# Kernel tuning notes

Hardware: AMD Instinct MI355X
Metric: run time of the kernel (lower is better)

Reference implementation:

```python
import jax, jax.numpy as jnp
import numpy as np

D_MODEL = 1024
NUM_HEADS = 16
THETA = 10000.0


def _rope(x, positions):
    # x: [..., S, d_k] with interleaved even/odd pairs; positions: [S] int
    d_k = x.shape[-1]
    inv_freq = 1.0 / (THETA ** (jnp.arange(0, d_k, 2, dtype=jnp.float32) / d_k))  # [d_k/2]
    freqs = positions.astype(jnp.float32)[:, None] * inv_freq[None, :]  # [S, d_k/2]
    cos = jnp.cos(freqs)
    sin = jnp.sin(freqs)
    x_even = x[..., 0::2]
    x_odd = x[..., 1::2]
    rot_even = x_even * cos - x_odd * sin
    rot_odd = x_even * sin + x_odd * cos
    out = jnp.stack([rot_even, rot_odd], axis=-1)  # [..., S, d_k/2, 2]
    return out.reshape(x.shape)


def setup_inputs() -> dict:
    key = jax.random.key(0)
    k1, k2, k3 = jax.random.split(key, 3)
    B, S = 2, 2048
    x = jax.random.normal(k1, (B, S, D_MODEL), dtype=jnp.float32)
    Wqkv = jax.random.normal(k2, (3 * D_MODEL, D_MODEL), dtype=jnp.float32) * (D_MODEL ** -0.5)
    Wout = jax.random.normal(k3, (D_MODEL, D_MODEL), dtype=jnp.float32) * (D_MODEL ** -0.5)
    token_positions = jnp.arange(S, dtype=jnp.int32)
    return {"x": x, "Wqkv": Wqkv, "Wout": Wout, "token_positions": token_positions}


def reference(x, Wqkv, Wout, token_positions):
    B, S, D = x.shape
    H = NUM_HEADS
    d_k = D // H
    qkv = x @ Wqkv.T  # [B, S, 3D]
    qkv = qkv.reshape(B, S, 3, H, d_k).transpose(0, 2, 3, 1, 4)  # [B, 3, H, S, d_k]
    q, k, v = qkv[:, 0], qkv[:, 1], qkv[:, 2]  # each [B, H, S, d_k]
    q = _rope(q, token_positions)
    k = _rope(k, token_positions)
    scores = jnp.einsum("bhqd,bhkd->bhqk", q, k) / jnp.sqrt(jnp.float32(d_k))
    attn = jax.nn.softmax(scores, axis=-1)
    out = jnp.einsum("bhqk,bhkd->bhqd", attn, v)  # [B, H, S, d_k]
    out = out.transpose(0, 2, 1, 3).reshape(B, S, D)
    return out @ Wout.T
```

## Files before the change

kernel.cpp:

```cpp
#include <hip/hip_runtime.h>
#include <stdint.h>

typedef unsigned short u16;
typedef unsigned int u32;
typedef __bf16 bf16x8 __attribute__((ext_vector_type(8)));
typedef float f32x4 __attribute__((ext_vector_type(4)));
typedef float f32x16 __attribute__((ext_vector_type(16)));

#define MFMA16 __builtin_amdgcn_mfma_f32_16x16x32_bf16
#define MFMA32 __builtin_amdgcn_mfma_f32_32x32x16_bf16

static __device__ __forceinline__ u16 f2bf(float f) {
  union { float f; u32 u; } v; v.f = f;
  u32 r = v.u + 0x7FFFu + ((v.u >> 16) & 1u);
  return (u16)(r >> 16);
}
static __device__ __forceinline__ float bf2f(u16 b) {
  union { float f; u32 u; } v; v.u = ((u32)b) << 16;
  return v.f;
}
static __device__ __forceinline__ void load_lds16(const void* g, void* l) {
  __builtin_amdgcn_global_load_lds(
      (const __attribute__((address_space(1))) void*)g,
      (__attribute__((address_space(3))) void*)l, 16, 0, 0);
}

__global__ __launch_bounds__(256) void cvt_bf16(const float* __restrict__ in,
                                                u16* __restrict__ out, int n4) {
  int i = blockIdx.x * 256 + threadIdx.x;
  if (i >= n4) return;
  float4 v = reinterpret_cast<const float4*>(in)[i];
  uint2 r;
  r.x = (u32)f2bf(v.x) | ((u32)f2bf(v.y) << 16);
  r.y = (u32)f2bf(v.z) | ((u32)f2bf(v.w) << 16);
  reinterpret_cast<uint2*>(out)[i] = r;
}

template <bool OUT_BF16>
__global__ __launch_bounds__(256, 2) void gemm_bt(const u16* __restrict__ A,
                                                  const u16* __restrict__ B,
                                                  void* __restrict__ Cv,
                                                  int M, int N, int K) {
  __shared__ u16 As[128 * 32];
  __shared__ u16 Bs[128 * 32];
  const int t = threadIdx.x;
  const int w = t >> 6, lane = t & 63;
  const int brow = blockIdx.y * 128, bcol = blockIdx.x * 128;
  const int wr = (w >> 1) * 64, wc = (w & 1) * 64;

  f32x4 acc[4][4];
#pragma unroll
  for (int i = 0; i < 4; ++i)
#pragma unroll
    for (int j = 0; j < 4; ++j) acc[i][j] = (f32x4){0.f, 0.f, 0.f, 0.f};

  const int srow = w * 16 + (lane >> 2);
  const int scol = (lane & 3) * 8;
  const u16* ga = A + (size_t)(brow + srow) * K + scol;
  const u16* gb = B + (size_t)(bcol + srow) * K + scol;
  const size_t rstep = (size_t)64 * K;
  u16* ldsA = As + w * 512;
  u16* ldsB = Bs + w * 512;

  const int lc = lane & 15, lg = lane >> 4;
  const int kg = lg * 8;

  const int nk = K >> 5;
  for (int kt = 0; kt < nk; ++kt) {
    __syncthreads();
    load_lds16(ga, ldsA);
    load_lds16(ga + rstep, (char*)ldsA + 4096);
    load_lds16(gb, ldsB);
    load_lds16(gb + rstep, (char*)ldsB + 4096);
    ga += 32; gb += 32;
    asm volatile("s_waitcnt vmcnt(0)" ::: "memory");
    __syncthreads();
    bf16x8 af[4], bfr[4];
#pragma unroll
    for (int i = 0; i < 4; ++i)
      af[i] = *reinterpret_cast<const bf16x8*>(As + (wr + i * 16 + lc) * 32 + kg);
#pragma unroll
    for (int j = 0; j < 4; ++j)
      bfr[j] = *reinterpret_cast<const bf16x8*>(Bs + (wc + j * 16 + lc) * 32 + kg);
#pragma unroll
    for (int i = 0; i < 4; ++i)
#pragma unroll
      for (int j = 0; j < 4; ++j)
        acc[i][j] = MFMA16(af[i], bfr[j], acc[i][j], 0, 0, 0);
  }

  const int r0 = lg * 4;
#pragma unroll
  for (int i = 0; i < 4; ++i)
#pragma unroll
    for (int j = 0; j < 4; ++j)
#pragma unroll
      for (int r = 0; r < 4; ++r) {
        const int m = brow + wr + i * 16 + r0 + r;
        const int n = bcol + wc + j * 16 + lc;
        if constexpr (OUT_BF16)
          ((u16*)Cv)[(size_t)m * N + n] = f2bf(acc[i][j][r]);
        else
          ((float*)Cv)[(size_t)m * N + n] = acc[i][j][r];
      }
}

__global__ __launch_bounds__(256) void build_trig(const int* __restrict__ pos,
                                                  float2* __restrict__ tab) {
  int i = blockIdx.x * 256 + threadIdx.x;
  int s = i >> 5, p = i & 31;
  float inv = powf(10000.0f, -(float)p * (1.0f / 32.0f));
  float fr = (float)pos[s] * inv;
  float sn, cs;
  sincosf(fr, &sn, &cs);
  tab[i] = make_float2(cs, sn);
}

__global__ __launch_bounds__(256) void rope_repack(const u16* __restrict__ qkv,
                                                   const float2* __restrict__ tab,
                                                   u16* __restrict__ Qro,
                                                   u16* __restrict__ Kro) {
  int idx = blockIdx.x * 256 + threadIdx.x;
  int p = idx & 31;
  int h = (idx >> 5) & 15;
  int m = idx >> 9;
  int b = m >> 11, s = m & 2047;
  const u32* row = reinterpret_cast<const u32*>(qkv + (size_t)m * 3072);
  u32 qp = row[h * 32 + p];
  u32 kp = row[512 + h * 32 + p];
  float2 cssn = tab[s * 32 + p];
  float cs = cssn.x, sn = cssn.y;
  float qe = bf2f((u16)(qp & 0xffffu)), qo = bf2f((u16)(qp >> 16));
  float ke = bf2f((u16)(kp & 0xffffu)), ko = bf2f((u16)(kp >> 16));
  const float QS = 0.18033688011112042f;
  float qre = (qe * cs - qo * sn) * QS;
  float qro_ = (qe * sn + qo * cs) * QS;
  float kre = ke * cs - ko * sn;
  float kro_ = ke * sn + ko * cs;
  size_t o = ((size_t)(b * 16 + h) * 2048 + s) * 32 + p;
  reinterpret_cast<u32*>(Qro)[o] = (u32)f2bf(qre) | ((u32)f2bf(qro_) << 16);
  reinterpret_cast<u32*>(Kro)[o] = (u32)f2bf(kre) | ((u32)f2bf(kro_) << 16);
}

__global__ __launch_bounds__(256) void v_transpose(const u16* __restrict__ qkv,
                                                   u16* __restrict__ VT) {
  const int bh = blockIdx.y;
  const int s0 = blockIdx.x * 64;
  const int b = bh >> 4, h = bh & 15;
  __shared__ u16 tile[64][72];
  const int t = threadIdx.x;
#pragma unroll
  for (int c = 0; c < 2; ++c) {
    int r = c * 32 + (t >> 3);
    int d = (t & 7) * 8;
    const u16* src = qkv + (size_t)(b * 2048 + s0 + r) * 3072 + 2048 + h * 64 + d;
    *reinterpret_cast<uint4*>(&tile[r][d]) = *reinterpret_cast<const uint4*>(src);
  }
  __syncthreads();
#pragma unroll
  for (int c = 0; c < 2; ++c) {
    int dd = c * 32 + (t >> 3);
    int sg = (t & 7) * 8;
    u16 tmp[8];
#pragma unroll
    for (int jj = 0; jj < 8; ++jj) tmp[jj] = tile[sg + jj][dd];
    *reinterpret_cast<uint4*>(VT + ((size_t)bh * 64 + dd) * 2048 + s0 + sg) =
        *reinterpret_cast<const uint4*>(tmp);
  }
}


static __device__ __forceinline__ void qk_tile(const char* lk,
                                               const bf16x8 (&qf)[4],
                                               f32x16 (&S)[2], int l31, int hi) {
#pragma unroll
  for (int i = 0; i < 2; ++i)
#pragma unroll
    for (int r = 0; r < 16; ++r) S[i][r] = 0.f;
  __builtin_amdgcn_s_setprio(1);
#pragma unroll
  for (int d = 0; d < 4; ++d) {
#pragma unroll
    for (int kvt = 0; kvt < 2; ++kvt) {
      int kv = kvt * 32 + l31;
      int a = (kv * 128 + d * 32 + hi * 16) ^ ((kv & 7) << 4);
      bf16x8 kf = *reinterpret_cast<const bf16x8*>(lk + a);
      S[kvt] = MFMA32(kf, qf[d], S[kvt], 0, 0, 0);
    }
  }
  __builtin_amdgcn_s_setprio(0);
}

static __device__ __forceinline__ void sm_pv(const char* lv, f32x16 (&SA)[2],
                                             f32x16 (&Oacc)[2], float& m,
                                             float& lsum, int l31, int hi) {
  float mt[16];
#pragma unroll
  for (int r = 0; r < 16; ++r) mt[r] = fmaxf(SA[0][r], SA[1][r]);
#pragma unroll
  for (int d = 8; d >= 1; d >>= 1)
#pragma unroll
    for (int r = 0; r < d; ++r) mt[r] = fmaxf(mt[r], mt[r + d]);
  float pmax = fmaxf(mt[0], __shfl_xor(mt[0], 32));

  if (__any(pmax > m + 6.0f)) {
    float mn = fmaxf(m, pmax);
    float sc = exp2f(m - mn);
    m = mn;
    lsum *= sc;
#pragma unroll
    for (int i = 0; i < 2; ++i)
#pragma unroll
      for (int r = 0; r < 16; ++r) Oacc[i][r] *= sc;
  }

#pragma unroll
  for (int kvt = 0; kvt < 2; ++kvt)
#pragma unroll
    for (int r = 0; r < 16; ++r) SA[kvt][r] = exp2f(SA[kvt][r] - m);

  {
    float st[16];
#pragma unroll
    for (int r = 0; r < 16; ++r) st[r] = SA[0][r] + SA[1][r];
#pragma unroll
    for (int d = 8; d >= 1; d >>= 1)
#pragma unroll
      for (int r = 0; r < d; ++r) st[r] += st[r + d];
    lsum += st[0];
  }

  bf16x8 pfrag[4];
#pragma unroll
  for (int kvt = 0; kvt < 2; ++kvt)
#pragma unroll
    for (int s1 = 0; s1 < 2; ++s1) {
      u32 X0, X1, Y0, Y1;
      const int c0 = s1 * 8, c1 = c0 + 4;
      asm("v_cvt_pk_bf16_f32 %0, %1, %2"
          : "=v"(X0) : "v"(SA[kvt][c0 + 0]), "v"(SA[kvt][c0 + 1]));
      asm("v_cvt_pk_bf16_f32 %0, %1, %2"
          : "=v"(X1) : "v"(SA[kvt][c0 + 2]), "v"(SA[kvt][c0 + 3]));
      asm("v_cvt_pk_bf16_f32 %0, %1, %2"
          : "=v"(Y0) : "v"(SA[kvt][c1 + 0]), "v"(SA[kvt][c1 + 1]));
      asm("v_cvt_pk_bf16_f32 %0, %1, %2"
          : "=v"(Y1) : "v"(SA[kvt][c1 + 2]), "v"(SA[kvt][c1 + 3]));
      asm("v_permlane32_swap_b32 %0, %1" : "+v"(X0), "+v"(Y0));
      asm("v_permlane32_swap_b32 %0, %1" : "+v"(X1), "+v"(Y1));
      union { u32 w[4]; bf16x8 v; } u;
      u.w[0] = X0; u.w[1] = X1; u.w[2] = Y0; u.w[3] = Y1;
      pfrag[kvt * 2 + s1] = u.v;
    }

  __builtin_amdgcn_s_setprio(1);
#pragma unroll
  for (int s = 0; s < 4; ++s) {
#pragma unroll
    for (int dt = 0; dt < 2; ++dt) {
      int d = dt * 32 + l31;
      int a = (d * 128 + s * 32 + hi * 16) ^ ((d & 7) << 4);
      bf16x8 vf = *reinterpret_cast<const bf16x8*>(lv + a);
      Oacc[dt] = MFMA32(vf, pfrag[s], Oacc[dt], 0, 0, 0);
    }
  }
  __builtin_amdgcn_s_setprio(0);
}

__global__ __launch_bounds__(256, 4) void attn_split(const u16* __restrict__ Q,
                                                     const u16* __restrict__ Kg,
                                                     const u16* __restrict__ VTg,
                                                     u16* __restrict__ part,
                                                     float2* __restrict__ stats) {
  constexpr int S = 2048, NT = 16;
  __shared__ char lds[2][16384];
  const int t = threadIdx.x, wv = t >> 6, lane = t & 63;
  const int bid = blockIdx.x;
  const int slot = bid >> 3;
  const int bh = (bid & 7) * 4 + (slot >> 5);
  const int rest = slot & 31;
  const int qb = rest >> 1, sp = rest & 1;
  const int q0 = qb * 128 + wv * 32;
  const size_t kbase = (size_t)bh * (S * 64);
  const int l31 = lane & 31, hi = lane >> 5;

  bf16x8 qf[4];
  {
    const u16* qp = Q + kbase + (size_t)(q0 + l31) * 64 + hi * 8;
#pragma unroll
    for (int d = 0; d < 4; ++d)
      qf[d] = *reinterpret_cast<const bf16x8*>(qp + d * 16);
  }

  f32x16 Oacc[2];
#pragma unroll
  for (int i = 0; i < 2; ++i)
#pragma unroll
    for (int r = 0; r < 16; ++r) Oacc[i][r] = 0.f;
  float m = -__builtin_inff(), lsum = 0.f;

  const char* gk0 = (const char*)(Kg + kbase);
  const char* gv0 = (const char*)(VTg + kbase);

#define STAGE(KT, BUF)                                                         \
  {                                                                            \
    char* lk_ = lds[BUF];                                                      \
    const char* gk_ = gk0 + (size_t)(sp * 16 + (KT)) * 8192;                   \
    _Pragma("unroll") for (int c_ = 0; c_ < 2; ++c_) {                         \
      int o_ = (c_ * 256 + t) * 16;                                            \
      int row_ = o_ >> 7, colb_ = o_ & 127;                                    \
      int swz_ = colb_ ^ ((row_ & 7) << 4);                                    \
      load_lds16(gk_ + row_ * 128 + swz_, lk_ + o_);                           \
      load_lds16(gv0 + (size_t)row_ * 4096 + sp * 2048 + (KT) * 128 + swz_,    \
                 lk_ + 8192 + o_);                                             \
    }                                                                          \
  }

  STAGE(0, 0)

  f32x16 Sa[2];
  for (int kt = 0; kt < NT; ++kt) {
    asm volatile("s_waitcnt vmcnt(0)" ::: "memory");
    __builtin_amdgcn_s_barrier();
    if (kt + 1 < NT) STAGE(kt + 1, (kt + 1) & 1)
    const char* lb = lds[kt & 1];
    qk_tile(lb, qf, Sa, l31, hi);
    sm_pv(lb + 8192, Sa, Oacc, m, lsum, l31, hi);
  }
#undef STAGE

  const float lfull = lsum + __shfl_xor(lsum, 32);
  const int srow = q0 + l31;
  const size_t rowi = (size_t)(sp * 32 + bh) * 2048 + srow;
  u16* prow = part + rowi * 64;
#pragma unroll
  for (int dt = 0; dt < 2; ++dt)
#pragma unroll
    for (int c = 0; c < 4; ++c) {
      uint2 pk;
      pk.x = (u32)f2bf(Oacc[dt][4 * c + 0]) | ((u32)f2bf(Oacc[dt][4 * c + 1]) << 16);
      pk.y = (u32)f2bf(Oacc[dt][4 * c + 2]) | ((u32)f2bf(Oacc[dt][4 * c + 3]) << 16);
      *reinterpret_cast<uint2*>(prow + dt * 32 + c * 8 + hi * 4) = pk;
    }
  if (hi == 0) stats[rowi] = make_float2(lfull, m);
}

__global__ __launch_bounds__(256) void attn_merge(const u16* __restrict__ part,
                                                  const float2* __restrict__ stats,
                                                  u16* __restrict__ attno) {
  int idx = blockIdx.x * 256 + threadIdx.x;
  int r = idx >> 3, c = idx & 7;
  float2 s0 = stats[r];
  float2 s1 = stats[65536 + r];
  float M = fmaxf(s0.y, s1.y);
  float w0 = exp2f(s0.y - M), w1 = exp2f(s1.y - M);
  float rden = 1.0f / (w0 * s0.x + w1 * s1.x);
  w0 *= rden; w1 *= rden;
  const uint4 a = *reinterpret_cast<const uint4*>(part + (size_t)r * 64 + c * 8);
  const uint4 b4 = *reinterpret_cast<const uint4*>(part + 4194304 + (size_t)r * 64 + c * 8);
  const u32 aw[4] = {a.x, a.y, a.z, a.w}, bw[4] = {b4.x, b4.y, b4.z, b4.w};
  u32 ow[4];
#pragma unroll
  for (int i = 0; i < 4; ++i) {
    float r0 = w0 * bf2f((u16)(aw[i] & 0xffffu)) + w1 * bf2f((u16)(bw[i] & 0xffffu));
    float r1 = w0 * bf2f((u16)(aw[i] >> 16)) + w1 * bf2f((u16)(bw[i] >> 16));
    ow[i] = (u32)f2bf(r0) | ((u32)f2bf(r1) << 16);
  }
  int bh = r >> 11, s = r & 2047;
  int b = bh >> 4, h = bh & 15;
  uint4 o; o.x = ow[0]; o.y = ow[1]; o.z = ow[2]; o.w = ow[3];
  *reinterpret_cast<uint4*>(attno + (size_t)(b * 2048 + s) * 1024 + h * 64 + c * 8) = o;
}

extern "C" void kernel_launch(void* const* d_in, const int* in_sizes, int n_in,
                              void* d_out, int out_size, void* d_ws, size_t ws_size,
                              hipStream_t stream) {
  (void)in_sizes; (void)n_in; (void)out_size; (void)ws_size;
  const float* x = (const float*)d_in[0];
  const float* wqkv = (const float*)d_in[1];
  const float* wout = (const float*)d_in[2];
  const int* pos = (const int*)d_in[3];
  float* out = (float*)d_out;

  char* ws = (char*)d_ws;
  u16* xb     = (u16*)(ws);
  u16* wqkvb  = (u16*)(ws + 8388608);
  u16* woutb  = (u16*)(ws + 14680064);
  u16* qkvb   = (u16*)(ws + 16777216);
  u16* qro    = (u16*)(ws + 41943040);
  u16* kro    = (u16*)(ws + 50331648);
  u16* vt     = (u16*)(ws + 58720256);
  u16* attno  = (u16*)(ws + 67108864);
  float2* tab = (float2*)(ws + 75497472);

  u16* part     = qkvb;
  float2* stats = (float2*)(ws + 16777216 + 16777216);

  cvt_bf16<<<4096, 256, 0, stream>>>(x, xb, 1048576);
  cvt_bf16<<<3072, 256, 0, stream>>>(wqkv, wqkvb, 786432);
  cvt_bf16<<<1024, 256, 0, stream>>>(wout, woutb, 262144);
  build_trig<<<256, 256, 0, stream>>>(pos, tab);
  gemm_bt<true><<<dim3(24, 32), 256, 0, stream>>>(xb, wqkvb, qkvb, 4096, 3072, 1024);
  rope_repack<<<8192, 256, 0, stream>>>(qkvb, tab, qro, kro);
  v_transpose<<<dim3(32, 32), 256, 0, stream>>>(qkvb, vt);
  attn_split<<<1024, 256, 0, stream>>>(qro, kro, vt, part, stats);
  attn_merge<<<2048, 256, 0, stream>>>(part, stats, attno);
  gemm_bt<false><<<dim3(8, 32), 256, 0, stream>>>(attno, woutb, out, 4096, 1024, 1024);
}
```

Measured before the change: 224.1 us.

## Fuse RoPE into QKV GEMM epilogue and merge prep kernels into one launch

The three bf16 conversion kernels and the trig-table build are merged into a single launch that dispatches on block index. The QKV GEMM epilogue now applies RoPE directly: it swaps even/odd pairs with a lane shuffle, applies the Q scale, and writes head-major Q/K. V goes to a separate packed buffer. This removes the rope_repack pass and the full QKV intermediate round trip through memory. In exchange, the GEMM epilogue does per-element table loads and scattered 2-byte stores, and the workspace layout is reshuffled.

```diff
diff --git a/kernel.cpp b/kernel.cpp
--- a/kernel.cpp
+++ b/kernel.cpp
@@ -25,22 +25,134 @@
       (__attribute__((address_space(3))) void*)l, 16, 0, 0);
 }
 
-__global__ __launch_bounds__(256) void cvt_bf16(const float* __restrict__ in,
-                                                u16* __restrict__ out, int n4) {
-  int i = blockIdx.x * 256 + threadIdx.x;
-  if (i >= n4) return;
-  float4 v = reinterpret_cast<const float4*>(in)[i];
-  uint2 r;
-  r.x = (u32)f2bf(v.x) | ((u32)f2bf(v.y) << 16);
-  r.y = (u32)f2bf(v.z) | ((u32)f2bf(v.w) << 16);
-  reinterpret_cast<uint2*>(out)[i] = r;
-}
-
-template <bool OUT_BF16>
-__global__ __launch_bounds__(256, 2) void gemm_bt(const u16* __restrict__ A,
-                                                  const u16* __restrict__ B,
-                                                  void* __restrict__ Cv,
-                                                  int M, int N, int K) {
+__global__ __launch_bounds__(256) void prep_fused(const float* __restrict__ x,
+                                                  const float* __restrict__ wqkv,
+                                                  const float* __restrict__ wout,
+                                                  const int* __restrict__ pos,
+                                                  u16* __restrict__ xb,
+                                                  u16* __restrict__ wqkvb,
+                                                  u16* __restrict__ woutb,
+                                                  float2* __restrict__ tab) {
+  const int blk = blockIdx.x;
+  if (blk < 8192) {
+    int i = blk * 256 + threadIdx.x;
+    const float* src;
+    u16* dst;
+    int off;
+    if (i < 1048576) { src = x; dst = xb; off = i; }
+    else if (i < 1835008) { src = wqkv; dst = wqkvb; off = i - 1048576; }
+    else { src = wout; dst = woutb; off = i - 1835008; }
+    float4 v = reinterpret_cast<const float4*>(src)[off];
+    uint2 r;
+    r.x = (u32)f2bf(v.x) | ((u32)f2bf(v.y) << 16);
+    r.y = (u32)f2bf(v.z) | ((u32)f2bf(v.w) << 16);
+    reinterpret_cast<uint2*>(dst)[off] = r;
+  } else {
+    int i = (blk - 8192) * 256 + threadIdx.x;
+    int s = i >> 5, p = i & 31;
+    float inv = powf(10000.0f, -(float)p * (1.0f / 32.0f));
+    float fr = (float)pos[s] * inv;
+    float sn, cs;
+    sincosf(fr, &sn, &cs);
+    tab[i] = make_float2(cs, sn);
+  }
+}
+
+__global__ __launch_bounds__(256, 2) void gemm_qkv(const u16* __restrict__ A,
+                                                   const u16* __restrict__ B,
+                                                   const float2* __restrict__ tab,
+                                                   u16* __restrict__ qro,
+                                                   u16* __restrict__ kro,
+                                                   u16* __restrict__ vpack) {
+  constexpr int K = 1024;
+  __shared__ u16 As[128 * 32];
+  __shared__ u16 Bs[128 * 32];
+  const int t = threadIdx.x;
+  const int w = t >> 6, lane = t & 63;
+  const int brow = blockIdx.y * 128, bcol = blockIdx.x * 128;
+  const int wr = (w >> 1) * 64, wc = (w & 1) * 64;
+
+  f32x4 acc[4][4];
+#pragma unroll
+  for (int i = 0; i < 4; ++i)
+#pragma unroll
+    for (int j = 0; j < 4; ++j) acc[i][j] = (f32x4){0.f, 0.f, 0.f, 0.f};
+
+  const int srow = w * 16 + (lane >> 2);
+  const int scol = (lane & 3) * 8;
+  const u16* ga = A + (size_t)(brow + srow) * K + scol;
+  const u16* gb = B + (size_t)(bcol + srow) * K + scol;
+  const size_t rstep = (size_t)64 * K;
+  u16* ldsA = As + w * 512;
+  u16* ldsB = Bs + w * 512;
+
+  const int lc = lane & 15, lg = lane >> 4;
+  const int kg = lg * 8;
+
+  for (int kt = 0; kt < K / 32; ++kt) {
+    __syncthreads();
+    load_lds16(ga, ldsA);
+    load_lds16(ga + rstep, (char*)ldsA + 4096);
+    load_lds16(gb, ldsB);
+    load_lds16(gb + rstep, (char*)ldsB + 4096);
+    ga += 32; gb += 32;
+    asm volatile("s_waitcnt vmcnt(0)" ::: "memory");
+    __syncthreads();
+    bf16x8 af[4], bfr[4];
+#pragma unroll
+    for (int i = 0; i < 4; ++i)
+      af[i] = *reinterpret_cast<const bf16x8*>(As + (wr + i * 16 + lc) * 32 + kg);
+#pragma unroll
+    for (int j = 0; j < 4; ++j)
+      bfr[j] = *reinterpret_cast<const bf16x8*>(Bs + (wc + j * 16 + lc) * 32 + kg);
+#pragma unroll
+    for (int i = 0; i < 4; ++i)
+#pragma unroll
+      for (int j = 0; j < 4; ++j)
+        acc[i][j] = MFMA16(af[i], bfr[j], acc[i][j], 0, 0, 0);
+  }
+
+  const int r0 = lg * 4;
+  if (bcol >= 2048) {
+#pragma unroll
+    for (int i = 0; i < 4; ++i)
+#pragma unroll
+      for (int j = 0; j < 4; ++j)
+#pragma unroll
+        for (int r = 0; r < 4; ++r) {
+          const int m = brow + wr + i * 16 + r0 + r;
+          const int n = bcol + wc + j * 16 + lc;
+          vpack[(size_t)m * 1024 + (n - 2048)] = f2bf(acc[i][j][r]);
+        }
+  } else {
+    const bool isq = bcol < 1024;
+    u16* dst = isq ? qro : kro;
+    const float scale = isq ? 0.18033688011112042f : 1.0f;
+#pragma unroll
+    for (int i = 0; i < 4; ++i)
+#pragma unroll
+      for (int j = 0; j < 4; ++j)
+#pragma unroll
+        for (int r = 0; r < 4; ++r) {
+          const int m = brow + wr + i * 16 + r0 + r;
+          const int n = bcol + wc + j * 16 + lc;
+          const int nn = n & 1023;
+          const int h = nn >> 6, d = nn & 63, p = d >> 1;
+          const int s = m & 2047, b = m >> 11;
+          float val = acc[i][j][r];
+          float pv = __shfl_xor(val, 1);
+          float2 cssn = tab[s * 32 + p];
+          float o = (d & 1) ? (pv * cssn.y + val * cssn.x)
+                            : (val * cssn.x - pv * cssn.y);
+          dst[((size_t)(b * 16 + h) * 2048 + s) * 64 + d] = f2bf(o * scale);
+        }
+  }
+}
+
+__global__ __launch_bounds__(256, 2) void gemm_out(const u16* __restrict__ A,
+                                                   const u16* __restrict__ B,
+                                                   float* __restrict__ C,
+                                                   int M, int N, int K) {
   __shared__ u16 As[128 * 32];
   __shared__ u16 Bs[128 * 32];
   const int t = threadIdx.x;
@@ -98,51 +210,11 @@
       for (int r = 0; r < 4; ++r) {
         const int m = brow + wr + i * 16 + r0 + r;
         const int n = bcol + wc + j * 16 + lc;
-        if constexpr (OUT_BF16)
-          ((u16*)Cv)[(size_t)m * N + n] = f2bf(acc[i][j][r]);
-        else
-          ((float*)Cv)[(size_t)m * N + n] = acc[i][j][r];
+        C[(size_t)m * N + n] = acc[i][j][r];
       }
 }
 
-__global__ __launch_bounds__(256) void build_trig(const int* __restrict__ pos,
-                                                  float2* __restrict__ tab) {
-  int i = blockIdx.x * 256 + threadIdx.x;
-  int s = i >> 5, p = i & 31;
-  float inv = powf(10000.0f, -(float)p * (1.0f / 32.0f));
-  float fr = (float)pos[s] * inv;
-  float sn, cs;
-  sincosf(fr, &sn, &cs);
-  tab[i] = make_float2(cs, sn);
-}
-
-__global__ __launch_bounds__(256) void rope_repack(const u16* __restrict__ qkv,
-                                                   const float2* __restrict__ tab,
-                                                   u16* __restrict__ Qro,
-                                                   u16* __restrict__ Kro) {
-  int idx = blockIdx.x * 256 + threadIdx.x;
-  int p = idx & 31;
-  int h = (idx >> 5) & 15;
-  int m = idx >> 9;
-  int b = m >> 11, s = m & 2047;
-  const u32* row = reinterpret_cast<const u32*>(qkv + (size_t)m * 3072);
-  u32 qp = row[h * 32 + p];
-  u32 kp = row[512 + h * 32 + p];
-  float2 cssn = tab[s * 32 + p];
-  float cs = cssn.x, sn = cssn.y;
-  float qe = bf2f((u16)(qp & 0xffffu)), qo = bf2f((u16)(qp >> 16));
-  float ke = bf2f((u16)(kp & 0xffffu)), ko = bf2f((u16)(kp >> 16));
-  const float QS = 0.18033688011112042f;
-  float qre = (qe * cs - qo * sn) * QS;
-  float qro_ = (qe * sn + qo * cs) * QS;
-  float kre = ke * cs - ko * sn;
-  float kro_ = ke * sn + ko * cs;
-  size_t o = ((size_t)(b * 16 + h) * 2048 + s) * 32 + p;
-  reinterpret_cast<u32*>(Qro)[o] = (u32)f2bf(qre) | ((u32)f2bf(qro_) << 16);
-  reinterpret_cast<u32*>(Kro)[o] = (u32)f2bf(kre) | ((u32)f2bf(kro_) << 16);
-}
-
-__global__ __launch_bounds__(256) void v_transpose(const u16* __restrict__ qkv,
+__global__ __launch_bounds__(256) void v_transpose(const u16* __restrict__ vpack,
                                                    u16* __restrict__ VT) {
   const int bh = blockIdx.y;
   const int s0 = blockIdx.x * 64;
@@ -153,7 +225,7 @@
   for (int c = 0; c < 2; ++c) {
     int r = c * 32 + (t >> 3);
     int d = (t & 7) * 8;
-    const u16* src = qkv + (size_t)(b * 2048 + s0 + r) * 3072 + 2048 + h * 64 + d;
+    const u16* src = vpack + (size_t)(b * 2048 + s0 + r) * 1024 + h * 64 + d;
     *reinterpret_cast<uint4*>(&tile[r][d]) = *reinterpret_cast<const uint4*>(src);
   }
   __syncthreads();
@@ -168,7 +240,6 @@
         *reinterpret_cast<const uint4*>(tmp);
   }
 }
-
 
 static __device__ __forceinline__ void qk_tile(const char* lk,
                                                const bf16x8 (&qf)[4],
@@ -385,24 +456,19 @@
   u16* xb     = (u16*)(ws);
   u16* wqkvb  = (u16*)(ws + 8388608);
   u16* woutb  = (u16*)(ws + 14680064);
-  u16* qkvb   = (u16*)(ws + 16777216);
+  u16* vpack  = (u16*)(ws + 16777216);
+  u16* part   = (u16*)(ws + 25165824);
   u16* qro    = (u16*)(ws + 41943040);
   u16* kro    = (u16*)(ws + 50331648);
   u16* vt     = (u16*)(ws + 58720256);
   u16* attno  = (u16*)(ws + 67108864);
   float2* tab = (float2*)(ws + 75497472);
-
-  u16* part     = qkvb;
-  float2* stats = (float2*)(ws + 16777216 + 16777216);
-
-  cvt_bf16<<<4096, 256, 0, stream>>>(x, xb, 1048576);
-  cvt_bf16<<<3072, 256, 0, stream>>>(wqkv, wqkvb, 786432);
-  cvt_bf16<<<1024, 256, 0, stream>>>(wout, woutb, 262144);
-  build_trig<<<256, 256, 0, stream>>>(pos, tab);
-  gemm_bt<true><<<dim3(24, 32), 256, 0, stream>>>(xb, wqkvb, qkvb, 4096, 3072, 1024);
-  rope_repack<<<8192, 256, 0, stream>>>(qkvb, tab, qro, kro);
-  v_transpose<<<dim3(32, 32), 256, 0, stream>>>(qkvb, vt);
+  float2* stats = (float2*)(ws);
+
+  prep_fused<<<8448, 256, 0, stream>>>(x, wqkv, wout, pos, xb, wqkvb, woutb, tab);
+  gemm_qkv<<<dim3(24, 32), 256, 0, stream>>>(xb, wqkvb, tab, qro, kro, vpack);
+  v_transpose<<<dim3(32, 32), 256, 0, stream>>>(vpack, vt);
   attn_split<<<1024, 256, 0, stream>>>(qro, kro, vt, part, stats);
   attn_merge<<<2048, 256, 0, stream>>>(part, stats, attno);
-  gemm_bt<false><<<dim3(8, 32), 256, 0, stream>>>(attno, woutb, out, 4096, 1024, 1024);
-}
+  gemm_out<<<dim3(8, 32), 256, 0, stream>>>(attno, woutb, out, 4096, 1024, 1024);
+}
```

New measurement: 215.0 us. 4.1% less time.
